# Performance work log

Measured on AMD Instinct MI355X. Metric: run time of the kernel, lower is better.

## Reference

```python
import jax, jax.numpy as jnp
import numpy as np

HIDDEN = 1024
HEADS = 16
HEAD_DIM = HIDDEN // HEADS


def setup_inputs() -> dict:
    key = jax.random.key(0)
    ks = jax.random.split(key, 9)
    B, S = 2, 2048
    std = 0.02
    inp = {
        "query": jax.random.normal(ks[0], (B, S, HIDDEN), dtype=jnp.float32),
        "Wq": jax.random.normal(ks[1], (HIDDEN, HIDDEN), dtype=jnp.float32) * std,
        "bq": jnp.zeros((HIDDEN,), dtype=jnp.float32),
        "Wk": jax.random.normal(ks[2], (HIDDEN, HIDDEN), dtype=jnp.float32) * std,
        "bk": jnp.zeros((HIDDEN,), dtype=jnp.float32),
        "Wv": jax.random.normal(ks[3], (HIDDEN, HIDDEN), dtype=jnp.float32) * std,
        "bv": jnp.zeros((HIDDEN,), dtype=jnp.float32),
        "Wo": jax.random.normal(ks[4], (HIDDEN, HIDDEN), dtype=jnp.float32) * std,
        "bo": jnp.zeros((HIDDEN,), dtype=jnp.float32),
    }
    return inp


def reference(query, Wq, bq, Wk, bk, Wv, bv, Wo, bo):
    B, S, H = query.shape
    # torch nn.Linear: y = x @ W.T + b
    Q = query @ Wq.T + bq
    K = query @ Wk.T + bk  # key defaults to query (self-attention)
    V = query @ Wv.T + bv
    # [B, S, H] -> [B, heads, S, head_dim]
    def split_heads(x):
        return x.reshape(B, S, HEADS, HEAD_DIM).transpose(0, 2, 1, 3)
    Qh, Kh, Vh = split_heads(Q), split_heads(K), split_heads(V)
    scale = jnp.sqrt(jnp.asarray(HEAD_DIM, dtype=query.dtype))
    scores = jnp.einsum("bhqd,bhkd->bhqk", Qh, Kh) / scale
    attn = jax.nn.softmax(scores, axis=-1)  # dropout=0 (eval)
    context = jnp.einsum("bhqk,bhkd->bhqd", attn, Vh)
    context = context.transpose(0, 2, 1, 3).reshape(B, S, H)
    output = context @ Wo.T + bo
    return output, attn
```

## Files before the change

kernel.cpp:

```cpp
#include <hip/hip_runtime.h>
#include <hip/hip_bf16.h>
#include <cstdint>

typedef __attribute__((ext_vector_type(4))) float f32x4;
typedef __attribute__((ext_vector_type(8))) short bf16x8;

__device__ __forceinline__ unsigned short f2bf(float f){
  union { float f; unsigned int u; } v; v.f = f;
  unsigned int u = v.u;
  u += 0x7FFFu + ((u >> 16) & 1u);
  return (unsigned short)(u >> 16);
}
__device__ __forceinline__ float bf2f(unsigned short s){
  union { unsigned int u; float f; } v; v.u = ((unsigned int)s) << 16;
  return v.f;
}

__global__ __launch_bounds__(256) void cvt_bf16(const float* __restrict__ in,
                                                unsigned short* __restrict__ out,
                                                int n4){
  int i = blockIdx.x * 256 + threadIdx.x;
  if (i < n4){
    float4 v = ((const float4*)in)[i];
    ushort4 o;
    o.x = f2bf(v.x); o.y = f2bf(v.y); o.z = f2bf(v.z); o.w = f2bf(v.w);
    ((ushort4*)out)[i] = o;
  }
}

__global__ __launch_bounds__(256) void qkv_gemm(
    const unsigned short* __restrict__ A,
    const unsigned short* __restrict__ W0,
    const unsigned short* __restrict__ W1,
    const unsigned short* __restrict__ W2,
    const float* __restrict__ b0,
    const float* __restrict__ b1,
    const float* __restrict__ b2,
    unsigned short* __restrict__ Qo,
    unsigned short* __restrict__ Khead,
    unsigned short* __restrict__ Vto)
{
  __shared__ unsigned short As[2][128*64];
  __shared__ unsigned short Bs[2][128*64];

  const int K = 1024;
  const int tid = threadIdx.x;
  const int l   = tid & 63;
  const int wid = tid >> 6;
  const int g   = l >> 4;
  const int li  = l & 15;
  const int widx = blockIdx.x >> 3;
  const int m0  = blockIdx.y * 128;
  const int n0  = (blockIdx.x & 7) * 128;
  const int wm  = (wid >> 1) * 64;
  const int wn  = (wid & 1) * 64;
  const int srow = tid >> 3;
  const int sck  = tid & 7;

  const unsigned short* Bw = (widx == 0) ? W0 : ((widx == 1) ? W1 : W2);
  const float* bias        = (widx == 0) ? b0 : ((widx == 1) ? b1 : b2);

  const unsigned short* Ag = A  + (size_t)(m0 + srow) * K + sck * 8;
  const unsigned short* Bg = Bw + (size_t)(n0 + srow) * K + sck * 8;

  f32x4 acc[4][4] = {};
  bf16x8 ra[4], rb[4];
  const int NT = K >> 6;

  #pragma unroll
  for (int r = 0; r < 4; ++r){
    ra[r] = *(const bf16x8*)(Ag + (size_t)(r*32) * K);
    rb[r] = *(const bf16x8*)(Bg + (size_t)(r*32) * K);
  }
  #pragma unroll
  for (int r = 0; r < 4; ++r){
    const int row = srow + r*32;
    const int ck  = sck ^ (row & 7);
    *(bf16x8*)(&As[0][row*64 + ck*8]) = ra[r];
    *(bf16x8*)(&Bs[0][row*64 + ck*8]) = rb[r];
  }
  __syncthreads();

  int cur = 0;
  for (int kt = 0; kt < NT; ++kt){
    if (kt + 1 < NT){
      const int kof = (kt + 1) << 6;
      #pragma unroll
      for (int r = 0; r < 4; ++r){
        ra[r] = *(const bf16x8*)(Ag + (size_t)(r*32) * K + kof);
        rb[r] = *(const bf16x8*)(Bg + (size_t)(r*32) * K + kof);
      }
    }
    #pragma unroll
    for (int kk = 0; kk < 2; ++kk){
      bf16x8 af[4], bfr[4];
      #pragma unroll
      for (int f = 0; f < 4; ++f){
        const int rowa = wm + f*16 + li;
        const int cka  = (kk*4 + g) ^ (rowa & 7);
        af[f] = *(const bf16x8*)(&As[cur][rowa*64 + cka*8]);
        const int rowb = wn + f*16 + li;
        const int ckb  = (kk*4 + g) ^ (rowb & 7);
        bfr[f] = *(const bf16x8*)(&Bs[cur][rowb*64 + ckb*8]);
      }
      #pragma unroll
      for (int fm = 0; fm < 4; ++fm)
        #pragma unroll
        for (int fn = 0; fn < 4; ++fn)
          acc[fm][fn] = __builtin_amdgcn_mfma_f32_16x16x32_bf16(af[fm], bfr[fn], acc[fm][fn], 0, 0, 0);
    }
    __syncthreads();
    if (kt + 1 < NT){
      #pragma unroll
      for (int r = 0; r < 4; ++r){
        const int row = srow + r*32;
        const int ck  = sck ^ (row & 7);
        *(bf16x8*)(&As[cur^1][row*64 + ck*8]) = ra[r];
        *(bf16x8*)(&Bs[cur^1][row*64 + ck*8]) = rb[r];
      }
      __syncthreads();
    }
    cur ^= 1;
  }

  #pragma unroll
  for (int fn = 0; fn < 4; ++fn){
    const int col = n0 + wn + fn*16 + li;
    const float bv = bias[col];
    #pragma unroll
    for (int fm = 0; fm < 4; ++fm){
      #pragma unroll
      for (int j = 0; j < 4; ++j){
        const int row = m0 + wm + fm*16 + g*4 + j;
        const float v = acc[fm][fn][j] + bv;
        const int bb = row >> 11;
        const int s  = row & 2047;
        if (widx == 0){
          Qo[(size_t)row * 1024 + col] = f2bf(v);
        } else if (widx == 1){
          const int hh = col >> 6, dd = col & 63;
          Khead[(((size_t)(bb*16 + hh))*2048 + s)*64 + dd] = f2bf(v);
        } else {
          Vto[((size_t)(bb*1024 + col)) * 2048 + s] = f2bf(v);
        }
      }
    }
  }
}

__global__ __launch_bounds__(256) void gemm_bt(
    const unsigned short* __restrict__ A,
    const unsigned short* __restrict__ Bw,
    const float* __restrict__ bias,
    float* __restrict__ outp,
    int M, int N, int K)
{
  __shared__ unsigned short As[2][128*64];
  __shared__ unsigned short Bs[2][128*64];

  const int tid = threadIdx.x;
  const int l   = tid & 63;
  const int wid = tid >> 6;
  const int g   = l >> 4;
  const int li  = l & 15;
  const int m0  = blockIdx.y * 128;
  const int n0  = blockIdx.x * 128;
  const int wm  = (wid >> 1) * 64;
  const int wn  = (wid & 1) * 64;
  const int srow = tid >> 3;
  const int sck  = tid & 7;

  const unsigned short* Ag = A  + (size_t)(m0 + srow) * K + sck * 8;
  const unsigned short* Bg = Bw + (size_t)(n0 + srow) * K + sck * 8;

  f32x4 acc[4][4] = {};
  bf16x8 ra[4], rb[4];
  const int NT = K >> 6;

  #pragma unroll
  for (int r = 0; r < 4; ++r){
    ra[r] = *(const bf16x8*)(Ag + (size_t)(r*32) * K);
    rb[r] = *(const bf16x8*)(Bg + (size_t)(r*32) * K);
  }
  #pragma unroll
  for (int r = 0; r < 4; ++r){
    const int row = srow + r*32;
    const int ck  = sck ^ (row & 7);
    *(bf16x8*)(&As[0][row*64 + ck*8]) = ra[r];
    *(bf16x8*)(&Bs[0][row*64 + ck*8]) = rb[r];
  }
  __syncthreads();

  int cur = 0;
  for (int kt = 0; kt < NT; ++kt){
    if (kt + 1 < NT){
      const int kof = (kt + 1) << 6;
      #pragma unroll
      for (int r = 0; r < 4; ++r){
        ra[r] = *(const bf16x8*)(Ag + (size_t)(r*32) * K + kof);
        rb[r] = *(const bf16x8*)(Bg + (size_t)(r*32) * K + kof);
      }
    }
    #pragma unroll
    for (int kk = 0; kk < 2; ++kk){
      bf16x8 af[4], bfr[4];
      #pragma unroll
      for (int f = 0; f < 4; ++f){
        const int rowa = wm + f*16 + li;
        const int cka  = (kk*4 + g) ^ (rowa & 7);
        af[f] = *(const bf16x8*)(&As[cur][rowa*64 + cka*8]);
        const int rowb = wn + f*16 + li;
        const int ckb  = (kk*4 + g) ^ (rowb & 7);
        bfr[f] = *(const bf16x8*)(&Bs[cur][rowb*64 + ckb*8]);
      }
      #pragma unroll
      for (int fm = 0; fm < 4; ++fm)
        #pragma unroll
        for (int fn = 0; fn < 4; ++fn)
          acc[fm][fn] = __builtin_amdgcn_mfma_f32_16x16x32_bf16(af[fm], bfr[fn], acc[fm][fn], 0, 0, 0);
    }
    __syncthreads();
    if (kt + 1 < NT){
      #pragma unroll
      for (int r = 0; r < 4; ++r){
        const int row = srow + r*32;
        const int ck  = sck ^ (row & 7);
        *(bf16x8*)(&As[cur^1][row*64 + ck*8]) = ra[r];
        *(bf16x8*)(&Bs[cur^1][row*64 + ck*8]) = rb[r];
      }
      __syncthreads();
    }
    cur ^= 1;
  }

  #pragma unroll
  for (int fn = 0; fn < 4; ++fn){
    const int col = n0 + wn + fn*16 + li;
    const float bv = bias[col];
    #pragma unroll
    for (int fm = 0; fm < 4; ++fm){
      #pragma unroll
      for (int j = 0; j < 4; ++j){
        const int row = m0 + wm + fm*16 + g*4 + j;
        outp[(size_t)row * N + col] = acc[fm][fn][j] + bv;
      }
    }
  }
}

__global__ __launch_bounds__(256, 2) void attn_all(
    const unsigned short* __restrict__ Qb,
    const unsigned short* __restrict__ Khead,
    const unsigned short* __restrict__ Vt,
    float* __restrict__ attn,
    unsigned short* __restrict__ ctxb)
{
  __shared__ __align__(16) char Kb8[256*144];
  __shared__ __align__(16) unsigned short Pw4[4][16*256];

  const int tid = threadIdx.x;
  const int l   = tid & 63;
  const int w   = tid >> 6;
  const int g   = l >> 4;
  const int li  = l & 15;
  const int bh  = blockIdx.x & 31;
  const int qt  = blockIdx.x >> 5;
  const int b   = bh >> 4;
  const int h   = bh & 15;

  const int qrow = qt*64 + w*16 + li;
  const size_t qoff = (size_t)(b*2048 + qrow) * 1024 + h*64 + g*8;
  const bf16x8 aq0 = *(const bf16x8*)(Qb + qoff);
  const bf16x8 aq1 = *(const bf16x8*)(Qb + qoff + 32);
  const unsigned short* Kg0 = Khead + (size_t)bh * (2048*64);

  float ls = 0.f;
  for (int kt = 0; kt < 8; ++kt){
    __syncthreads();
    {
      const unsigned short* Kg = Kg0 + (size_t)kt * (256*64);
      #pragma unroll
      for (int p = 0; p < 8; ++p){
        const int key = p*32 + (tid >> 3);
        const int c   = tid & 7;
        const bf16x8 v = *(const bf16x8*)(Kg + (size_t)key*64 + c*8);
        *(bf16x8*)(Kb8 + key*144 + ((c ^ (key & 7)) * 16)) = v;
      }
    }
    __syncthreads();
    #pragma unroll
    for (int cf = 0; cf < 16; ++cf){
      const int key = cf*16 + li;
      const bf16x8 k0 = *(const bf16x8*)(Kb8 + key*144 + (( g    ^ (key & 7)) * 16));
      const bf16x8 k1 = *(const bf16x8*)(Kb8 + key*144 + (((g+4) ^ (key & 7)) * 16));
      f32x4 t = {};
      t = __builtin_amdgcn_mfma_f32_16x16x32_bf16(k0, aq0, t, 0, 0, 0);
      t = __builtin_amdgcn_mfma_f32_16x16x32_bf16(k1, aq1, t, 0, 0, 0);
      ls += __expf(t[0]*0.125f) + __expf(t[1]*0.125f)
          + __expf(t[2]*0.125f) + __expf(t[3]*0.125f);
    }
  }
  ls += __shfl_xor(ls, 16);
  ls += __shfl_xor(ls, 32);
  const float rv = 1.0f / ls;

  f32x4 pv[4] = {};
  char* myP = (char*)(&Pw4[w][0]);
  const int swz = (li & 7) << 3;
  const unsigned short* Vb0 = Vt + (size_t)(b*1024 + h*64) * 2048;
  float* arow0 = attn + ((size_t)bh*2048 + qt*64 + w*16) * 2048;

  for (int kt = 0; kt < 8; ++kt){
    __syncthreads();
    {
      const unsigned short* Kg = Kg0 + (size_t)kt * (256*64);
      #pragma unroll
      for (int p = 0; p < 8; ++p){
        const int key = p*32 + (tid >> 3);
        const int c   = tid & 7;
        const bf16x8 v = *(const bf16x8*)(Kg + (size_t)key*64 + c*8);
        *(bf16x8*)(Kb8 + key*144 + ((c ^ (key & 7)) * 16)) = v;
      }
    }
    __syncthreads();

    #pragma unroll
    for (int cf = 0; cf < 16; ++cf){
      const int key = cf*16 + li;
      const bf16x8 k0 = *(const bf16x8*)(Kb8 + key*144 + (( g    ^ (key & 7)) * 16));
      const bf16x8 k1 = *(const bf16x8*)(Kb8 + key*144 + (((g+4) ^ (key & 7)) * 16));
      f32x4 t = {};
      t = __builtin_amdgcn_mfma_f32_16x16x32_bf16(k0, aq0, t, 0, 0, 0);
      t = __builtin_amdgcn_mfma_f32_16x16x32_bf16(k1, aq1, t, 0, 0, 0);
      ushort4 u;
      u.x = f2bf(__expf(t[0]*0.125f) * rv);
      u.y = f2bf(__expf(t[1]*0.125f) * rv);
      u.z = f2bf(__expf(t[2]*0.125f) * rv);
      u.w = f2bf(__expf(t[3]*0.125f) * rv);
      *(ushort4*)(myP + li*512 + ((cf*32 + g*8) ^ swz)) = u;
    }

    #pragma unroll
    for (int vh = 0; vh < 2; ++vh){
      bf16x8 vb[16];
      #pragma unroll
      for (int ks = 0; ks < 4; ++ks)
        #pragma unroll
        for (int df = 0; df < 4; ++df)
          vb[ks*4+df] = *(const bf16x8*)(Vb0 + (size_t)(df*16 + li)*2048
                                         + kt*256 + (vh*4+ks)*32 + g*8);
      #pragma unroll
      for (int ks = 0; ks < 4; ++ks){
        const int colb = (vh*4+ks)*64 + g*16;
        const ushort4 plo = *(const ushort4*)(myP + li*512 + ( colb      ^ swz));
        const ushort4 phi = *(const ushort4*)(myP + li*512 + ((colb + 8) ^ swz));
        bf16x8 pa;
        pa[0] = plo.x; pa[1] = plo.y; pa[2] = plo.z; pa[3] = plo.w;
        pa[4] = phi.x; pa[5] = phi.y; pa[6] = phi.z; pa[7] = phi.w;
        #pragma unroll
        for (int df = 0; df < 4; ++df)
          pv[df] = __builtin_amdgcn_mfma_f32_16x16x32_bf16(pa, vb[ks*4+df], pv[df], 0, 0, 0);
      }
    }

    #pragma unroll
    for (int r = 0; r < 16; ++r){
      const ushort4 u = *(const ushort4*)(myP + r*512 + ((l*8) ^ ((r & 7) << 3)));
      f32x4 o;
      o[0] = bf2f(u.x); o[1] = bf2f(u.y); o[2] = bf2f(u.z); o[3] = bf2f(u.w);
      __builtin_nontemporal_store(o, (f32x4*)(arow0 + (size_t)r*2048 + kt*256 + l*4));
    }
  }

  #pragma unroll
  for (int df = 0; df < 4; ++df)
    #pragma unroll
    for (int j = 0; j < 4; ++j)
      ctxb[(size_t)(b*2048 + qt*64 + w*16 + g*4 + j)*1024 + h*64 + df*16 + li]
        = f2bf(pv[df][j]);
}

extern "C" void kernel_launch(void* const* d_in, const int* in_sizes, int n_in,
                              void* d_out, int out_size, void* d_ws, size_t ws_size,
                              hipStream_t stream)
{
  const float* X  = (const float*)d_in[0];
  const float* Wq = (const float*)d_in[1];
  const float* bq = (const float*)d_in[2];
  const float* Wk = (const float*)d_in[3];
  const float* bk = (const float*)d_in[4];
  const float* Wv = (const float*)d_in[5];
  const float* bv = (const float*)d_in[6];
  const float* Wo = (const float*)d_in[7];
  const float* bo = (const float*)d_in[8];

  char* ws = (char*)d_ws;
  unsigned short* Xb    = (unsigned short*)(ws);
  unsigned short* Qb    = (unsigned short*)(ws + (size_t)( 8u<<20));
  unsigned short* Khead = (unsigned short*)(ws + (size_t)(16u<<20));
  unsigned short* Vt    = (unsigned short*)(ws + (size_t)(24u<<20));
  unsigned short* Cb    = (unsigned short*)(ws + (size_t)(32u<<20));
  unsigned short* Wqb   = (unsigned short*)(ws + (size_t)(40u<<20));
  unsigned short* Wkb   = (unsigned short*)(ws + (size_t)(42u<<20));
  unsigned short* Wvb   = (unsigned short*)(ws + (size_t)(44u<<20));
  unsigned short* Wob   = (unsigned short*)(ws + (size_t)(46u<<20));

  float* out  = (float*)d_out;
  float* attn = out + (size_t)4194304;

  cvt_bf16<<<4096, 256, 0, stream>>>(X,  Xb,  1048576);
  cvt_bf16<<<1024, 256, 0, stream>>>(Wq, Wqb, 262144);
  cvt_bf16<<<1024, 256, 0, stream>>>(Wk, Wkb, 262144);
  cvt_bf16<<<1024, 256, 0, stream>>>(Wv, Wvb, 262144);
  cvt_bf16<<<1024, 256, 0, stream>>>(Wo, Wob, 262144);

  dim3 qkvgrid(24, 32);
  qkv_gemm<<<qkvgrid, 256, 0, stream>>>(Xb, Wqb, Wkb, Wvb, bq, bk, bv, Qb, Khead, Vt);

  attn_all<<<dim3(1024), 256, 0, stream>>>(Qb, Khead, Vt, attn, Cb);

  dim3 ggrid(8, 32);
  gemm_bt<<<ggrid, 256, 0, stream>>>(Cb, Wob, bo, out, 4096, 1024, 1024);
}
```

Baseline: 338.8 us.

## Warp-specialize attention: split row-sum pass and offload attn writes to extra waves

The attention kernel now runs 512 threads per block. In the first pass, the two groups of four waves split the key tiles by parity and combine their partial row sums through shared memory. In the second pass, waves 0-3 compute P and P·V into a double-buffered shared P tile, while waves 4-7 stream the previous tile's probabilities out to the fp32 attention matrix. This is meant to overlap the large attn writes with MFMA work and to halve the redundant row-sum compute per wave. In exchange it uses more shared memory and registers per block, which may reduce occupancy.

```diff
diff --git a/kernel.cpp b/kernel.cpp
--- a/kernel.cpp
+++ b/kernel.cpp
@@ -248,7 +248,7 @@
   }
 }
 
-__global__ __launch_bounds__(256, 2) void attn_all(
+__global__ __launch_bounds__(512, 2) void attn_all(
     const unsigned short* __restrict__ Qb,
     const unsigned short* __restrict__ Khead,
     const unsigned short* __restrict__ Vt,
@@ -256,11 +256,13 @@
     unsigned short* __restrict__ ctxb)
 {
   __shared__ __align__(16) char Kb8[256*144];
-  __shared__ __align__(16) unsigned short Pw4[4][16*256];
+  __shared__ __align__(16) unsigned short Pw4[4][2][16*256];
+  __shared__ float red[128];
 
   const int tid = threadIdx.x;
   const int l   = tid & 63;
   const int w   = tid >> 6;
+  const int cw  = w & 3;
   const int g   = l >> 4;
   const int li  = l & 15;
   const int bh  = blockIdx.x & 31;
@@ -268,55 +270,59 @@
   const int b   = bh >> 4;
   const int h   = bh & 15;
 
-  const int qrow = qt*64 + w*16 + li;
+  const int qrow = qt*64 + cw*16 + li;
   const size_t qoff = (size_t)(b*2048 + qrow) * 1024 + h*64 + g*8;
   const bf16x8 aq0 = *(const bf16x8*)(Qb + qoff);
   const bf16x8 aq1 = *(const bf16x8*)(Qb + qoff + 32);
   const unsigned short* Kg0 = Khead + (size_t)bh * (2048*64);
 
+  const int parity = w >> 2;
   float ls = 0.f;
   for (int kt = 0; kt < 8; ++kt){
     __syncthreads();
     {
       const unsigned short* Kg = Kg0 + (size_t)kt * (256*64);
       #pragma unroll
-      for (int p = 0; p < 8; ++p){
-        const int key = p*32 + (tid >> 3);
+      for (int p = 0; p < 4; ++p){
+        const int key = p*64 + (tid >> 3);
         const int c   = tid & 7;
         const bf16x8 v = *(const bf16x8*)(Kg + (size_t)key*64 + c*8);
         *(bf16x8*)(Kb8 + key*144 + ((c ^ (key & 7)) * 16)) = v;
       }
     }
     __syncthreads();
-    #pragma unroll
-    for (int cf = 0; cf < 16; ++cf){
-      const int key = cf*16 + li;
-      const bf16x8 k0 = *(const bf16x8*)(Kb8 + key*144 + (( g    ^ (key & 7)) * 16));
-      const bf16x8 k1 = *(const bf16x8*)(Kb8 + key*144 + (((g+4) ^ (key & 7)) * 16));
-      f32x4 t = {};
-      t = __builtin_amdgcn_mfma_f32_16x16x32_bf16(k0, aq0, t, 0, 0, 0);
-      t = __builtin_amdgcn_mfma_f32_16x16x32_bf16(k1, aq1, t, 0, 0, 0);
-      ls += __expf(t[0]*0.125f) + __expf(t[1]*0.125f)
-          + __expf(t[2]*0.125f) + __expf(t[3]*0.125f);
+    if ((kt & 1) == parity){
+      #pragma unroll
+      for (int cf = 0; cf < 16; ++cf){
+        const int key = cf*16 + li;
+        const bf16x8 k0 = *(const bf16x8*)(Kb8 + key*144 + (( g    ^ (key & 7)) * 16));
+        const bf16x8 k1 = *(const bf16x8*)(Kb8 + key*144 + (((g+4) ^ (key & 7)) * 16));
+        f32x4 t = {};
+        t = __builtin_amdgcn_mfma_f32_16x16x32_bf16(k0, aq0, t, 0, 0, 0);
+        t = __builtin_amdgcn_mfma_f32_16x16x32_bf16(k1, aq1, t, 0, 0, 0);
+        ls += __expf(t[0]*0.125f) + __expf(t[1]*0.125f)
+            + __expf(t[2]*0.125f) + __expf(t[3]*0.125f);
+      }
     }
   }
   ls += __shfl_xor(ls, 16);
   ls += __shfl_xor(ls, 32);
-  const float rv = 1.0f / ls;
+  if (l < 16) red[w*16 + l] = ls;
+  __syncthreads();
+  const float rv = 1.0f / (red[cw*16 + li] + red[(cw+4)*16 + li]);
 
   f32x4 pv[4] = {};
-  char* myP = (char*)(&Pw4[w][0]);
   const int swz = (li & 7) << 3;
   const unsigned short* Vb0 = Vt + (size_t)(b*1024 + h*64) * 2048;
-  float* arow0 = attn + ((size_t)bh*2048 + qt*64 + w*16) * 2048;
+  float* arow0 = attn + ((size_t)bh*2048 + qt*64 + cw*16) * 2048;
 
   for (int kt = 0; kt < 8; ++kt){
     __syncthreads();
     {
       const unsigned short* Kg = Kg0 + (size_t)kt * (256*64);
       #pragma unroll
-      for (int p = 0; p < 8; ++p){
-        const int key = p*32 + (tid >> 3);
+      for (int p = 0; p < 4; ++p){
+        const int key = p*64 + (tid >> 3);
         const int c   = tid & 7;
         const bf16x8 v = *(const bf16x8*)(Kg + (size_t)key*64 + c*8);
         *(bf16x8*)(Kb8 + key*144 + ((c ^ (key & 7)) * 16)) = v;
@@ -324,60 +330,75 @@
     }
     __syncthreads();
 
-    #pragma unroll
-    for (int cf = 0; cf < 16; ++cf){
-      const int key = cf*16 + li;
-      const bf16x8 k0 = *(const bf16x8*)(Kb8 + key*144 + (( g    ^ (key & 7)) * 16));
-      const bf16x8 k1 = *(const bf16x8*)(Kb8 + key*144 + (((g+4) ^ (key & 7)) * 16));
-      f32x4 t = {};
-      t = __builtin_amdgcn_mfma_f32_16x16x32_bf16(k0, aq0, t, 0, 0, 0);
-      t = __builtin_amdgcn_mfma_f32_16x16x32_bf16(k1, aq1, t, 0, 0, 0);
-      ushort4 u;
-      u.x = f2bf(__expf(t[0]*0.125f) * rv);
-      u.y = f2bf(__expf(t[1]*0.125f) * rv);
-      u.z = f2bf(__expf(t[2]*0.125f) * rv);
-      u.w = f2bf(__expf(t[3]*0.125f) * rv);
-      *(ushort4*)(myP + li*512 + ((cf*32 + g*8) ^ swz)) = u;
-    }
-
-    #pragma unroll
-    for (int vh = 0; vh < 2; ++vh){
-      bf16x8 vb[16];
-      #pragma unroll
-      for (int ks = 0; ks < 4; ++ks)
+    if (w < 4){
+      char* myP = (char*)(&Pw4[cw][kt & 1][0]);
+      #pragma unroll
+      for (int cf = 0; cf < 16; ++cf){
+        const int key = cf*16 + li;
+        const bf16x8 k0 = *(const bf16x8*)(Kb8 + key*144 + (( g    ^ (key & 7)) * 16));
+        const bf16x8 k1 = *(const bf16x8*)(Kb8 + key*144 + (((g+4) ^ (key & 7)) * 16));
+        f32x4 t = {};
+        t = __builtin_amdgcn_mfma_f32_16x16x32_bf16(k0, aq0, t, 0, 0, 0);
+        t = __builtin_amdgcn_mfma_f32_16x16x32_bf16(k1, aq1, t, 0, 0, 0);
+        ushort4 u;
+        u.x = f2bf(__expf(t[0]*0.125f) * rv);
+        u.y = f2bf(__expf(t[1]*0.125f) * rv);
+        u.z = f2bf(__expf(t[2]*0.125f) * rv);
+        u.w = f2bf(__expf(t[3]*0.125f) * rv);
+        *(ushort4*)(myP + li*512 + ((cf*32 + g*8) ^ swz)) = u;
+      }
+      #pragma unroll
+      for (int vh = 0; vh < 2; ++vh){
+        bf16x8 vb[16];
         #pragma unroll
-        for (int df = 0; df < 4; ++df)
-          vb[ks*4+df] = *(const bf16x8*)(Vb0 + (size_t)(df*16 + li)*2048
-                                         + kt*256 + (vh*4+ks)*32 + g*8);
-      #pragma unroll
-      for (int ks = 0; ks < 4; ++ks){
-        const int colb = (vh*4+ks)*64 + g*16;
-        const ushort4 plo = *(const ushort4*)(myP + li*512 + ( colb      ^ swz));
-        const ushort4 phi = *(const ushort4*)(myP + li*512 + ((colb + 8) ^ swz));
-        bf16x8 pa;
-        pa[0] = plo.x; pa[1] = plo.y; pa[2] = plo.z; pa[3] = plo.w;
-        pa[4] = phi.x; pa[5] = phi.y; pa[6] = phi.z; pa[7] = phi.w;
+        for (int ks = 0; ks < 4; ++ks)
+          #pragma unroll
+          for (int df = 0; df < 4; ++df)
+            vb[ks*4+df] = *(const bf16x8*)(Vb0 + (size_t)(df*16 + li)*2048
+                                           + kt*256 + (vh*4+ks)*32 + g*8);
         #pragma unroll
-        for (int df = 0; df < 4; ++df)
-          pv[df] = __builtin_amdgcn_mfma_f32_16x16x32_bf16(pa, vb[ks*4+df], pv[df], 0, 0, 0);
-      }
-    }
-
+        for (int ks = 0; ks < 4; ++ks){
+          const int colb = (vh*4+ks)*64 + g*16;
+          const ushort4 plo = *(const ushort4*)(myP + li*512 + ( colb      ^ swz));
+          const ushort4 phi = *(const ushort4*)(myP + li*512 + ((colb + 8) ^ swz));
+          bf16x8 pa;
+          pa[0] = plo.x; pa[1] = plo.y; pa[2] = plo.z; pa[3] = plo.w;
+          pa[4] = phi.x; pa[5] = phi.y; pa[6] = phi.z; pa[7] = phi.w;
+          #pragma unroll
+          for (int df = 0; df < 4; ++df)
+            pv[df] = __builtin_amdgcn_mfma_f32_16x16x32_bf16(pa, vb[ks*4+df], pv[df], 0, 0, 0);
+        }
+      }
+    } else if (kt > 0){
+      const char* pP = (const char*)(&Pw4[cw][(kt-1) & 1][0]);
+      #pragma unroll
+      for (int r = 0; r < 16; ++r){
+        const ushort4 u = *(const ushort4*)(pP + r*512 + ((l*8) ^ ((r & 7) << 3)));
+        f32x4 o;
+        o[0] = bf2f(u.x); o[1] = bf2f(u.y); o[2] = bf2f(u.z); o[3] = bf2f(u.w);
+        __builtin_nontemporal_store(o, (f32x4*)(arow0 + (size_t)r*2048 + (kt-1)*256 + l*4));
+      }
+    }
+  }
+
+  __syncthreads();
+  if (w >= 4){
+    const char* pP = (const char*)(&Pw4[cw][1][0]);
     #pragma unroll
     for (int r = 0; r < 16; ++r){
-      const ushort4 u = *(const ushort4*)(myP + r*512 + ((l*8) ^ ((r & 7) << 3)));
+      const ushort4 u = *(const ushort4*)(pP + r*512 + ((l*8) ^ ((r & 7) << 3)));
       f32x4 o;
       o[0] = bf2f(u.x); o[1] = bf2f(u.y); o[2] = bf2f(u.z); o[3] = bf2f(u.w);
-      __builtin_nontemporal_store(o, (f32x4*)(arow0 + (size_t)r*2048 + kt*256 + l*4));
-    }
-  }
-
-  #pragma unroll
-  for (int df = 0; df < 4; ++df)
-    #pragma unroll
-    for (int j = 0; j < 4; ++j)
-      ctxb[(size_t)(b*2048 + qt*64 + w*16 + g*4 + j)*1024 + h*64 + df*16 + li]
-        = f2bf(pv[df][j]);
+      __builtin_nontemporal_store(o, (f32x4*)(arow0 + (size_t)r*2048 + 7*256 + l*4));
+    }
+  } else {
+    #pragma unroll
+    for (int df = 0; df < 4; ++df)
+      #pragma unroll
+      for (int j = 0; j < 4; ++j)
+        ctxb[(size_t)(b*2048 + qt*64 + cw*16 + g*4 + j)*1024 + h*64 + df*16 + li]
+          = f2bf(pv[df][j]);
+  }
 }
 
 extern "C" void kernel_launch(void* const* d_in, const int* in_sizes, int n_in,
@@ -417,7 +438,7 @@
   dim3 qkvgrid(24, 32);
   qkv_gemm<<<qkvgrid, 256, 0, stream>>>(Xb, Wqb, Wkb, Wvb, bq, bk, bv, Qb, Khead, Vt);
 
-  attn_all<<<dim3(1024), 256, 0, stream>>>(Qb, Khead, Vt, attn, Cb);
+  attn_all<<<dim3(1024), 512, 0, stream>>>(Qb, Khead, Vt, attn, Cb);
 
   dim3 ggrid(8, 32);
   gemm_bt<<<ggrid, 256, 0, stream>>>(Cb, Wob, bo, out, 4096, 1024, 1024);
```

New measurement: 333.6 us. Within noise of the previous version (-1.5%).
